# Performance work log

Measured on AMD Instinct MI355X. Metric: run time of the kernel, lower is better.

Reference implementation:

```python
import jax, jax.numpy as jnp
import numpy as np

B, D, F, K, C = 1024, 768, 24576, 64, 32  # tokens, act dim, dict size, topk, conns/feature


def setup_inputs() -> dict:
    key = jax.random.key(0)
    ks = jax.random.split(key, 9)
    s = 1.0 / np.sqrt(D)
    inp = {
        "x_up": jax.random.normal(ks[0], (B, D), jnp.float32),
        "x_down": jax.random.normal(ks[1], (B, D), jnp.float32),
        "W_enc_up": jax.random.normal(ks[2], (F, D), jnp.float32) * s,
        "b_enc_up": jnp.zeros((F,), jnp.float32),
        "W_dec_up": jax.random.normal(ks[3], (D, F), jnp.float32) * s,
        "b_dec_up": jnp.zeros((D,), jnp.float32),
        "W_enc_down": jax.random.normal(ks[4], (F, D), jnp.float32) * s,
        "b_enc_down": jnp.zeros((F,), jnp.float32),
        "W_dec_down": jax.random.normal(ks[5], (D, F), jnp.float32) * s,
        "b_dec_down": jnp.zeros((D,), jnp.float32),
    }
    # sparse adjacency: indices of connected upstream features, -1 padded
    conn = jax.random.randint(ks[6], (F, C), 0, F)
    drop = jax.random.uniform(ks[7], (F, C)) < 0.25
    inp["connections"] = jnp.where(drop, -1, conn).astype(jnp.int64)
    return inp


def _encode_topk(x, W_enc, b_enc, b_dec):
    # AutoEncoderTopK.encode: relu(Linear(x - b_dec)) then top-k, scatter to dense
    pre = jnp.maximum((x - b_dec) @ W_enc.T + b_enc, 0.0)  # [B, F]
    top_vals, top_idx = jax.lax.top_k(pre, K)              # [B, K]
    feats = jnp.zeros_like(pre).at[jnp.arange(x.shape[0])[:, None], top_idx].set(top_vals)
    return feats, top_vals, top_idx


def _decode(f, W_dec, b_dec):
    return f @ W_dec.T + b_dec


def _contributions(connections, W_dec_up, W_enc_down, up_idx, down_idx, up_vals):
    # get_virtual_weights: gather connection rows, match against active upstream
    allowed_up = connections[down_idx]                      # [B, Kd, C]
    valid = allowed_up != -1
    # match[b, kd, c, ku] = allowed_up==up_idx (masked); sum over c -> multiplicity
    match = (allowed_up[..., None] == up_idx[:, None, None, :]) & valid[..., None]
    count = match.sum(axis=2).astype(up_vals.dtype)         # [B, Kd, Ku]
    down_rows = W_enc_down[down_idx]                        # [B, Kd, D]
    up_cols = W_dec_up.T[up_idx]                            # [B, Ku, D]
    vw = jnp.einsum('bkd,bud->bku', down_rows, up_cols)     # virtual weights
    return jnp.einsum('bku,bku,bu->bk', vw, count, up_vals)  # [B, Kd]


def reference(x_up, x_down, W_enc_up, b_enc_up, W_dec_up, b_dec_up,
              W_enc_down, b_enc_down, W_dec_down, b_dec_down, connections):
    # vanilla forward (upstream recon + topk info for both)
    feats_up, up_vals, up_idx = _encode_topk(x_up, W_enc_up, b_enc_up, b_dec_up)
    recon_up = _decode(feats_up, W_dec_up, b_dec_up)
    _, down_vals, down_idx = _encode_topk(x_down, W_enc_down, b_enc_down, b_dec_down)
    # approx_forward: downstream activations approximated from virtual weights
    approx_acts = _contributions(connections, W_dec_up, W_enc_down, up_idx, down_idx, up_vals)
    approx_feats = jnp.zeros((x_down.shape[0], F), x_down.dtype).at[
        jnp.arange(x_down.shape[0])[:, None], down_idx].set(approx_acts)
    recon_down = _decode(approx_feats, W_dec_down, b_dec_down)
    return jnp.stack([recon_up, recon_down])  # [2, B, D]
```

## Files before the change

kernel.cpp:

```cpp
#include <hip/hip_runtime.h>
#include <hip/hip_bf16.h>

#define TPB 256

typedef __attribute__((ext_vector_type(4))) float f32x4;
typedef __bf16 bf16x8 __attribute__((ext_vector_type(8)));

__device__ __forceinline__ void gload16(const bf16x8* g, bf16x8* l) {
  __builtin_amdgcn_global_load_lds(
      (const __attribute__((address_space(1))) unsigned int*)g,
      (__attribute__((address_space(3))) unsigned int*)l, 16, 0, 0);
}

__device__ __forceinline__ double dot_w64(const double* xs, const float* wr,
                                          int lane, int D) {
  double sum = 0.0;
  if ((D >> 6) == 12) {
    float wv[12];
#pragma unroll
    for (int u = 0; u < 12; ++u) wv[u] = wr[lane + (u << 6)];
#pragma unroll
    for (int u = 0; u < 12; ++u) sum += xs[lane + (u << 6)] * (double)wv[u];
  } else {
    for (int d = lane; d < D; d += 64) sum += xs[d] * (double)wr[d];
  }
#pragma unroll
  for (int m = 32; m > 0; m >>= 1) sum += __shfl_xor(sum, m, 64);
  return sum;
}

__device__ __forceinline__ float dotf_w64(const float* a, const float* b,
                                          int lane, int D) {
  float s = 0.f;
  if ((D >> 6) == 12) {
    float av[12], bv[12];
#pragma unroll
    for (int u = 0; u < 12; ++u) {
      av[u] = a[lane + (u << 6)];
      bv[u] = b[lane + (u << 6)];
    }
#pragma unroll
    for (int u = 0; u < 12; ++u) s += av[u] * bv[u];
  } else {
    for (int d = lane; d < D; d += 64) s += a[d] * b[d];
  }
#pragma unroll
  for (int m = 32; m > 0; m >>= 1) s += __shfl_xor(s, m, 64);
  return s;
}

__global__ __launch_bounds__(TPB) void pack_tiles(
    const float* __restrict__ src, const float* __restrict__ sub,
    bf16x8* __restrict__ dst, int D) {
  const int r0 = blockIdx.x * 128;
  const int k0 = blockIdx.y * 32;
  const size_t tile = ((size_t)blockIdx.x * gridDim.y + blockIdx.y) * 512;
#pragma unroll
  for (int e = 0; e < 2; ++e) {
    const int q = e * 256 + threadIdx.x;
    const int row = q & 127, g = q >> 7;
    const float* s = src + (size_t)(r0 + row) * D + k0 + g * 8;
    f32x4 v0 = *(const f32x4*)s;
    f32x4 v1 = *(const f32x4*)(s + 4);
    if (sub) {
      const float* bp = sub + k0 + g * 8;
      v0 = v0 - *(const f32x4*)bp;
      v1 = v1 - *(const f32x4*)(bp + 4);
    }
    bf16x8 o;
#pragma unroll
    for (int u = 0; u < 4; ++u) o[u] = (__bf16)v0[u];
#pragma unroll
    for (int u = 0; u < 4; ++u) o[u + 4] = (__bf16)v1[u];
    dst[tile + q] = o;
  }
}

__global__ __launch_bounds__(TPB) void enc_gemm_bf(
    const bf16x8* __restrict__ A,
    const bf16x8* __restrict__ W,
    const float* __restrict__ benc,
    __bf16* __restrict__ pre,
    int nkt, int F) {
  __shared__ bf16x8 As[512], Ws[512];
  const int t = threadIdx.x;
  const int lane = t & 63, wv = t >> 6;
  const int wm = (wv >> 1) * 64, wn = (wv & 1) * 64;
  const int lrow = lane & 15, quad = lane >> 4;
  const size_t Ab = (size_t)blockIdx.y * nkt * 512;
  const size_t Wb = (size_t)blockIdx.x * nkt * 512;

  f32x4 acc[4][4];
#pragma unroll
  for (int i = 0; i < 4; ++i)
#pragma unroll
    for (int j = 0; j < 4; ++j) acc[i][j] = (f32x4){0.f, 0.f, 0.f, 0.f};

  for (int kt = 0; kt < nkt; ++kt) {
    __syncthreads();
    const bf16x8* ag = A + Ab + (size_t)kt * 512 + wv * 128;
    const bf16x8* wg = W + Wb + (size_t)kt * 512 + wv * 128;
    bf16x8* al = As + wv * 128;
    bf16x8* wl = Ws + wv * 128;
    gload16(ag + lane, al);
    gload16(ag + 64 + lane, al + 64);
    gload16(wg + lane, wl);
    gload16(wg + 64 + lane, wl + 64);
    __syncthreads();
    bf16x8 af[4];
#pragma unroll
    for (int i = 0; i < 4; ++i) af[i] = As[quad * 128 + wm + i * 16 + lrow];
#pragma unroll
    for (int j = 0; j < 4; ++j) {
      bf16x8 bfr = Ws[quad * 128 + wn + j * 16 + lrow];
#pragma unroll
      for (int i = 0; i < 4; ++i)
        acc[i][j] = __builtin_amdgcn_mfma_f32_16x16x32_bf16(af[i], bfr, acc[i][j], 0, 0, 0);
    }
  }
  const int bf0 = blockIdx.x * 128, bb = blockIdx.y * 128;
#pragma unroll
  for (int j = 0; j < 4; ++j) {
    const int col = bf0 + wn + j * 16 + lrow;
    const float bc = benc[col];
#pragma unroll
    for (int i = 0; i < 4; ++i) {
      const int row0 = bb + wm + i * 16 + quad * 4;
#pragma unroll
      for (int rg = 0; rg < 4; ++rg) {
        float v = acc[i][j][rg] + bc;
        v = v > 0.f ? v : 0.f;
        pre[(size_t)(row0 + rg) * F + col] = (__bf16)v;
      }
    }
  }
}

#define TK_CAP 2048
#define BAND_CAP 256
#define TK_EPS 0.06f

__global__ __launch_bounds__(TPB) void topk_sel(
    const unsigned short* __restrict__ pre,
    const float* __restrict__ x, const float* __restrict__ W,
    const float* __restrict__ benc, const float* __restrict__ bdec,
    float* __restrict__ vals, int* __restrict__ idxs,
    int D, int F) {
  const int b = blockIdx.x;
  const int tid = threadIdx.x;
  const unsigned short* row = pre + (size_t)b * F;

  __shared__ float cval[TK_CAP];
  __shared__ int cidx[TK_CAP];
  __shared__ unsigned hist[256];
  __shared__ double xs[768];
  __shared__ int bcand[BAND_CAP];
  __shared__ double bexact[BAND_CAP];
  __shared__ int sh_cnt, sh_out, sh_band;
  __shared__ float sh_thr;
  __shared__ unsigned sh_prefix, sh_need;

  for (int d = tid; d < D; d += TPB)
    xs[d] = (double)x[(size_t)b * D + d] - (double)bdec[d];
  if (tid == 0) sh_thr = 1.75f;
  __syncthreads();

  int n;
  float T;
  for (;;) {
    if (tid == 0) sh_cnt = 0;
    __syncthreads();
    const float thr = sh_thr;
    for (int i = tid * 8; i < F; i += TPB * 8) {
      uint4 pk = *(const uint4*)(row + i);
      unsigned wbits[4] = {pk.x, pk.y, pk.z, pk.w};
#pragma unroll
      for (int u = 0; u < 4; ++u) {
        float v0 = __uint_as_float((wbits[u] & 0xFFFFu) << 16);
        float v1 = __uint_as_float(wbits[u] & 0xFFFF0000u);
        if (v0 > thr) {
          int p = atomicAdd(&sh_cnt, 1);
          if (p < TK_CAP) { cval[p] = v0; cidx[p] = i + 2 * u; }
        }
        if (v1 > thr) {
          int p = atomicAdd(&sh_cnt, 1);
          if (p < TK_CAP) { cval[p] = v1; cidx[p] = i + 2 * u + 1; }
        }
      }
    }
    __syncthreads();
    n = sh_cnt;
    if (n >= 64 && n <= TK_CAP) {
      if (tid == 0) { sh_prefix = 0u; sh_need = 64u; }
      __syncthreads();
      for (int pass = 0; pass < 4; ++pass) {
        const int shift = 24 - 8 * pass;
        hist[tid] = 0u;
        __syncthreads();
        const unsigned prefix = sh_prefix;
        const unsigned maskhi = (pass == 0) ? 0u : (0xFFFFFFFFu << (shift + 8));
        for (int q = tid; q < n; q += TPB) {
          unsigned k = __float_as_uint(cval[q]);
          if ((k & maskhi) == prefix) atomicAdd(&hist[(k >> shift) & 255], 1u);
        }
        __syncthreads();
        if (tid == 0) {
          unsigned need = sh_need, cum = 0;
          int bsel = 0;
          for (int bin = 255; bin >= 0; --bin) {
            if (cum + hist[bin] >= need) { bsel = bin; break; }
            cum += hist[bin];
          }
          sh_prefix = prefix | ((unsigned)bsel << shift);
          sh_need = need - cum;
        }
        __syncthreads();
      }
      T = __uint_as_float(sh_prefix);
      if (thr < T - TK_EPS) break;
      if (tid == 0) sh_thr = T - 2.f * TK_EPS;
    } else {
      if (tid == 0) sh_thr = (n < 64) ? fmaxf(thr - 0.75f, 1e-3f) : thr + 0.75f;
    }
    __syncthreads();
  }

  if (tid == 0) { sh_out = 0; sh_band = 0; }
  __syncthreads();
  const float hicut = T + TK_EPS, locut = T - TK_EPS;
  float* ovals = vals + (size_t)b * 64;
  int* oidx = idxs + (size_t)b * 64;
  for (int q = tid; q < n; q += TPB) {
    const float v = cval[q];
    if (v > hicut) {
      int p = atomicAdd(&sh_out, 1);
      ovals[p] = v; oidx[p] = cidx[q];
    } else if (v >= locut) {
      int p = atomicAdd(&sh_band, 1);
      if (p < BAND_CAP) bcand[p] = cidx[q];
    }
  }
  __syncthreads();
  const int s = sh_out;
  const int bn = sh_band < BAND_CAP ? sh_band : BAND_CAP;
  const int needk = 64 - s;
  const int lane = tid & 63, wv = tid >> 6;
  for (int q = wv; q < bn; q += 4) {
    double sum = dot_w64(xs, W + (size_t)bcand[q] * D, lane, D);
    if (lane == 0) {
      double v = sum + (double)benc[bcand[q]];
      bexact[q] = v > 0.0 ? v : 0.0;
    }
  }
  __syncthreads();
  if (tid < bn) {
    const double v = bexact[tid];
    const int id = bcand[tid];
    int rank = 0;
    for (int j = 0; j < bn; ++j)
      rank += (bexact[j] > v) || (bexact[j] == v && bcand[j] < id);
    if (rank < needk) { ovals[s + rank] = (float)v; oidx[s + rank] = id; }
  }
}

__global__ __launch_bounds__(TPB) void transpose_df(
    const float* __restrict__ in, float* __restrict__ out, int D, int F) {
  __shared__ float tile[32][33];
  const int f0 = blockIdx.x * 32;
  const int d0 = blockIdx.y * 32;
  const int tx = threadIdx.x & 31;
  const int ty = threadIdx.x >> 5;
#pragma unroll
  for (int i = 0; i < 4; ++i)
    tile[ty + i * 8][tx] = in[(size_t)(d0 + ty + i * 8) * F + f0 + tx];
  __syncthreads();
#pragma unroll
  for (int i = 0; i < 4; ++i)
    out[(size_t)(f0 + ty + i * 8) * D + d0 + tx] = tile[tx][ty + i * 8];
}

__global__ __launch_bounds__(TPB) void decode64(
    const float* __restrict__ WT, const float* __restrict__ bdec,
    const float* __restrict__ vals, const int* __restrict__ idxs,
    float* __restrict__ out, int D) {
  const int b = blockIdx.x;
  __shared__ float sv[64];
  __shared__ int si[64];
  const int tid = threadIdx.x;
  if (tid < 64) {
    sv[tid] = vals[(size_t)b * 64 + tid];
    si[tid] = idxs[(size_t)b * 64 + tid];
  }
  __syncthreads();
  const int nd4 = D >> 2;
  for (int d4 = tid; d4 < nd4; d4 += TPB) {
    f32x4 acc = *(const f32x4*)(bdec + d4 * 4);
#pragma unroll 8
    for (int k = 0; k < 64; ++k)
      acc += *(const f32x4*)(WT + (size_t)si[k] * D + d4 * 4) * sv[k];
    *(f32x4*)(out + (size_t)b * D + d4 * 4) = acc;
  }
}

__global__ __launch_bounds__(TPB) void contrib(
    const int* __restrict__ conn, const float* __restrict__ Wencd,
    const float* __restrict__ WTdecu,
    const float* __restrict__ up_vals, const int* __restrict__ up_idx,
    const int* __restrict__ down_idx,
    float* __restrict__ approx, int D, int C) {
  const int b = blockIdx.x;
  __shared__ int sui[64];
  __shared__ float suv[64];
  __shared__ int sdi[64];
  __shared__ float sacc[64];
  __shared__ int queue[2048];
  __shared__ int qn;
  const int tid = threadIdx.x;
  if (tid < 64) {
    sui[tid] = up_idx[(size_t)b * 64 + tid];
    suv[tid] = up_vals[(size_t)b * 64 + tid];
    sdi[tid] = down_idx[(size_t)b * 64 + tid];
    sacc[tid] = 0.0f;
  }
  if (tid == 0) qn = 0;
  __syncthreads();
  const int npairs = 64 * C;
  for (int p = tid; p < npairs; p += TPB) {
    int kd = p / C, c = p - kd * C;
    int f = conn[(size_t)sdi[kd] * C + c];
    if (f < 0) continue;
    for (int ku = 0; ku < 64; ++ku) {
      if (sui[ku] == f) {
        int q = atomicAdd(&qn, 1);
        queue[q] = (kd << 8) | ku;
        break;
      }
    }
  }
  __syncthreads();
  const int n = qn;
  const int lane = tid & 63, wv = tid >> 6;
  for (int q = wv; q < n; q += 4) {
    const int kd = queue[q] >> 8, ku = queue[q] & 255;
    float s = dotf_w64(Wencd + (size_t)sdi[kd] * D,
                       WTdecu + (size_t)sui[ku] * D, lane, D);
    if (lane == 0) atomicAdd(&sacc[kd], suv[ku] * s);
  }
  __syncthreads();
  if (tid < 64) approx[(size_t)b * 64 + tid] = sacc[tid];
}

extern "C" void kernel_launch(void* const* d_in, const int* in_sizes, int n_in,
                              void* d_out, int out_size, void* d_ws, size_t ws_size,
                              hipStream_t stream) {
  const float* x_up   = (const float*)d_in[0];
  const float* x_down = (const float*)d_in[1];
  const float* Wenc_u = (const float*)d_in[2];
  const float* benc_u = (const float*)d_in[3];
  const float* Wdec_u = (const float*)d_in[4];
  const float* bdec_u = (const float*)d_in[5];
  const float* Wenc_d = (const float*)d_in[6];
  const float* benc_d = (const float*)d_in[7];
  const float* Wdec_d = (const float*)d_in[8];
  const float* bdec_d = (const float*)d_in[9];
  const int*   conn   = (const int*)d_in[10];

  const int D = in_sizes[5];
  const int B = in_sizes[0] / D;
  const int F = in_sizes[3];
  const int C = in_sizes[10] / F;
  const int nkt = D / 32;

  float* out = (float*)d_out;
  char* w = (char*)d_ws;

  __bf16* pre16 = (__bf16*)w;
  bf16x8* Wperm = (bf16x8*)(w + (size_t)B * F * 2);
  bf16x8* xuP   = (bf16x8*)(w + (size_t)B * F * 2 + (size_t)F * D * 2);
  bf16x8* xdP   = xuP + (size_t)B * D / 8;
  float* up_vals = (float*)(xdP + (size_t)B * D / 8);
  int*   up_idx  = (int*)(up_vals + (size_t)B * 64);
  float* dn_vals = (float*)(up_idx + (size_t)B * 64);
  int*   dn_idx  = (int*)(dn_vals + (size_t)B * 64);
  float* approx  = (float*)(dn_idx + (size_t)B * 64);
  float* WT = (float*)w;

  dim3 packW_grid(F / 128, nkt);
  dim3 packX_grid(B / 128, nkt);
  dim3 gemm_grid(F / 128, B / 128);
  dim3 tr_grid(F / 32, D / 32);

  pack_tiles<<<packX_grid, TPB, 0, stream>>>(x_up, bdec_u, xuP, D);
  pack_tiles<<<packW_grid, TPB, 0, stream>>>(Wenc_u, nullptr, Wperm, D);
  enc_gemm_bf<<<gemm_grid, TPB, 0, stream>>>(xuP, Wperm, benc_u, pre16, nkt, F);
  topk_sel<<<B, TPB, 0, stream>>>((const unsigned short*)pre16, x_up, Wenc_u,
                                  benc_u, bdec_u, up_vals, up_idx, D, F);
  pack_tiles<<<packX_grid, TPB, 0, stream>>>(x_down, bdec_d, xdP, D);
  pack_tiles<<<packW_grid, TPB, 0, stream>>>(Wenc_d, nullptr, Wperm, D);
  enc_gemm_bf<<<gemm_grid, TPB, 0, stream>>>(xdP, Wperm, benc_d, pre16, nkt, F);
  topk_sel<<<B, TPB, 0, stream>>>((const unsigned short*)pre16, x_down, Wenc_d,
                                  benc_d, bdec_d, dn_vals, dn_idx, D, F);

  transpose_df<<<tr_grid, TPB, 0, stream>>>(Wdec_u, WT, D, F);
  decode64<<<B, TPB, 0, stream>>>(WT, bdec_u, up_vals, up_idx, out, D);
  contrib<<<B, TPB, 0, stream>>>(conn, Wenc_d, WT, up_vals, up_idx, dn_idx,
                                 approx, D, C);
  transpose_df<<<tr_grid, TPB, 0, stream>>>(Wdec_d, WT, D, F);
  decode64<<<B, TPB, 0, stream>>>(WT, bdec_d, approx, dn_idx, out + (size_t)B * D, D);
}
```

Before: 693.7 us.

## Fuse top-k candidate collection into encoder GEMM epilogue

The encoder GEMM epilogue now compares each bf16 activation against a fixed threshold and appends a packed (value bits, column) word to a per-row global candidate list via atomics. The first pack kernel zeroes the counters. The top-k kernel reads that list instead of rescanning the full pre-activation row. Only if the count is out of range does it fall back to rescanning, now with a halving threshold step. The radix select uses packed keys, runs two passes instead of four, and finds the bin with a wave-level scan instead of a serial loop on one thread. This costs global atomics and scattered writes in the GEMM epilogue.

```diff
diff --git a/kernel.cpp b/kernel.cpp
--- a/kernel.cpp
+++ b/kernel.cpp
@@ -2,9 +2,17 @@
 #include <hip/hip_bf16.h>
 
 #define TPB 256
+#define TK_CAP 2048
+#define BAND_CAP 256
+#define TK_EPS 0.06f
+#define TK_THR 1.75f
 
 typedef __attribute__((ext_vector_type(4))) float f32x4;
 typedef __bf16 bf16x8 __attribute__((ext_vector_type(8)));
+
+__device__ __forceinline__ unsigned short bf16_bits(__bf16 h) {
+  return __builtin_bit_cast(unsigned short, h);
+}
 
 __device__ __forceinline__ void gload16(const bf16x8* g, bf16x8* l) {
   __builtin_amdgcn_global_load_lds(
@@ -51,7 +59,9 @@
 
 __global__ __launch_bounds__(TPB) void pack_tiles(
     const float* __restrict__ src, const float* __restrict__ sub,
-    bf16x8* __restrict__ dst, int D) {
+    bf16x8* __restrict__ dst, int D, unsigned* __restrict__ cntz, int nrows) {
+  if (cntz && blockIdx.x == 0 && blockIdx.y == 0)
+    for (int i = threadIdx.x; i < nrows; i += TPB) cntz[i] = 0u;
   const int r0 = blockIdx.x * 128;
   const int k0 = blockIdx.y * 32;
   const size_t tile = ((size_t)blockIdx.x * gridDim.y + blockIdx.y) * 512;
@@ -81,6 +91,8 @@
     const bf16x8* __restrict__ W,
     const float* __restrict__ benc,
     __bf16* __restrict__ pre,
+    unsigned* __restrict__ cnt,
+    unsigned* __restrict__ cand,
     int nkt, int F) {
   __shared__ bf16x8 As[512], Ws[512];
   const int t = threadIdx.x;
@@ -130,98 +142,133 @@
       for (int rg = 0; rg < 4; ++rg) {
         float v = acc[i][j][rg] + bc;
         v = v > 0.f ? v : 0.f;
-        pre[(size_t)(row0 + rg) * F + col] = (__bf16)v;
+        const __bf16 hb = (__bf16)v;
+        pre[(size_t)(row0 + rg) * F + col] = hb;
+        const unsigned ub = (unsigned)bf16_bits(hb);
+        const float vb = __uint_as_float(ub << 16);
+        if (vb > TK_THR) {
+          const int r = row0 + rg;
+          const unsigned p = atomicAdd(&cnt[r], 1u);
+          if (p < TK_CAP) cand[(size_t)r * TK_CAP + p] = (ub << 16) | (unsigned)col;
+        }
       }
     }
   }
 }
 
-#define TK_CAP 2048
-#define BAND_CAP 256
-#define TK_EPS 0.06f
-
-__global__ __launch_bounds__(TPB) void topk_sel(
+__global__ __launch_bounds__(TPB) void topk_sel2(
+    const unsigned* __restrict__ cnt, const unsigned* __restrict__ cand,
     const unsigned short* __restrict__ pre,
     const float* __restrict__ x, const float* __restrict__ W,
     const float* __restrict__ benc, const float* __restrict__ bdec,
-    float* __restrict__ vals, int* __restrict__ idxs,
-    int D, int F) {
+    float* __restrict__ vals, int* __restrict__ idxs, int D, int F) {
   const int b = blockIdx.x;
   const int tid = threadIdx.x;
-  const unsigned short* row = pre + (size_t)b * F;
-
-  __shared__ float cval[TK_CAP];
-  __shared__ int cidx[TK_CAP];
+
+  __shared__ unsigned cpack[TK_CAP];
   __shared__ unsigned hist[256];
   __shared__ double xs[768];
   __shared__ int bcand[BAND_CAP];
   __shared__ double bexact[BAND_CAP];
   __shared__ int sh_cnt, sh_out, sh_band;
+  __shared__ unsigned sh_prefix, sh_need;
   __shared__ float sh_thr;
-  __shared__ unsigned sh_prefix, sh_need;
 
   for (int d = tid; d < D; d += TPB)
     xs[d] = (double)x[(size_t)b * D + d] - (double)bdec[d];
-  if (tid == 0) sh_thr = 1.75f;
-  __syncthreads();
-
-  int n;
-  float T;
-  for (;;) {
-    if (tid == 0) sh_cnt = 0;
-    __syncthreads();
-    const float thr = sh_thr;
-    for (int i = tid * 8; i < F; i += TPB * 8) {
-      uint4 pk = *(const uint4*)(row + i);
-      unsigned wbits[4] = {pk.x, pk.y, pk.z, pk.w};
-#pragma unroll
-      for (int u = 0; u < 4; ++u) {
-        float v0 = __uint_as_float((wbits[u] & 0xFFFFu) << 16);
-        float v1 = __uint_as_float(wbits[u] & 0xFFFF0000u);
-        if (v0 > thr) {
-          int p = atomicAdd(&sh_cnt, 1);
-          if (p < TK_CAP) { cval[p] = v0; cidx[p] = i + 2 * u; }
+
+  int n = 0;
+  bool have = false;
+  {
+    const int nc = (int)cnt[b];
+    if (nc >= 64 && nc <= TK_CAP) {
+      for (int q = tid; q < nc; q += TPB) cpack[q] = cand[(size_t)b * TK_CAP + q];
+      n = nc;
+      have = true;
+    }
+  }
+  if (tid == 0) sh_thr = TK_THR;
+  __syncthreads();
+
+  float T = 0.f;
+  float step = 0.375f;
+  for (int outer = 0; outer < 40; ++outer) {
+    if (!have) {
+      const unsigned short* row = pre + (size_t)b * F;
+      for (int tries = 0; tries < 40; ++tries) {
+        if (tid == 0) sh_cnt = 0;
+        __syncthreads();
+        const float thr = sh_thr;
+        for (int i = tid * 8; i < F; i += TPB * 8) {
+          const uint4 pk = *(const uint4*)(row + i);
+          const unsigned wb[4] = {pk.x, pk.y, pk.z, pk.w};
+#pragma unroll
+          for (int u = 0; u < 4; ++u) {
+            const unsigned lo = wb[u] << 16;
+            const unsigned hi = wb[u] & 0xFFFF0000u;
+            if (__uint_as_float(lo) > thr) {
+              int p = atomicAdd(&sh_cnt, 1);
+              if (p < TK_CAP) cpack[p] = lo | (unsigned)(i + 2 * u);
+            }
+            if (__uint_as_float(hi) > thr) {
+              int p = atomicAdd(&sh_cnt, 1);
+              if (p < TK_CAP) cpack[p] = hi | (unsigned)(i + 2 * u + 1);
+            }
+          }
         }
-        if (v1 > thr) {
-          int p = atomicAdd(&sh_cnt, 1);
-          if (p < TK_CAP) { cval[p] = v1; cidx[p] = i + 2 * u + 1; }
+        __syncthreads();
+        n = sh_cnt;
+        if (n >= 64 && n <= TK_CAP) break;
+        if (tid == 0) sh_thr = (n < 64) ? sh_thr - step : sh_thr + step;
+        step *= 0.5f;
+        __syncthreads();
+      }
+      if (n > TK_CAP) n = TK_CAP;
+    }
+
+    if (tid == 0) { sh_prefix = 0u; sh_need = 64u; }
+#pragma unroll
+    for (int pass = 0; pass < 2; ++pass) {
+      const int shift = 24 - 8 * pass;
+      hist[tid] = 0u;
+      __syncthreads();
+      const unsigned prefix = sh_prefix;
+      const unsigned maskhi = pass == 0 ? 0u : 0xFF000000u;
+      for (int q = tid; q < n; q += TPB) {
+        const unsigned k = cpack[q];
+        if ((k & maskhi) == prefix) atomicAdd(&hist[(k >> shift) & 255u], 1u);
+      }
+      __syncthreads();
+      if (tid < 64) {
+        const unsigned h0 = hist[tid * 4], h1 = hist[tid * 4 + 1];
+        const unsigned h2 = hist[tid * 4 + 2], h3 = hist[tid * 4 + 3];
+        const unsigned lsum = h0 + h1 + h2 + h3;
+        unsigned s = lsum;
+#pragma unroll
+        for (int off = 1; off < 64; off <<= 1) {
+          const unsigned o = __shfl_down(s, off, 64);
+          if (tid + off < 64) s += o;
+        }
+        const unsigned above = s - lsum;
+        const unsigned t3 = h3, t2 = h2 + t3, t1 = h1 + t2, t0 = h0 + t1;
+        const unsigned suf[4] = {above + t0, above + t1, above + t2, above + t3};
+        const unsigned hh[4] = {h0, h1, h2, h3};
+        const unsigned need = sh_need;
+#pragma unroll
+        for (int u = 0; u < 4; ++u) {
+          if (suf[u] >= need && suf[u] - hh[u] < need) {
+            sh_prefix = prefix | ((unsigned)(tid * 4 + u) << shift);
+            sh_need = need - (suf[u] - hh[u]);
+          }
         }
       }
-    }
-    __syncthreads();
-    n = sh_cnt;
-    if (n >= 64 && n <= TK_CAP) {
-      if (tid == 0) { sh_prefix = 0u; sh_need = 64u; }
       __syncthreads();
-      for (int pass = 0; pass < 4; ++pass) {
-        const int shift = 24 - 8 * pass;
-        hist[tid] = 0u;
-        __syncthreads();
-        const unsigned prefix = sh_prefix;
-        const unsigned maskhi = (pass == 0) ? 0u : (0xFFFFFFFFu << (shift + 8));
-        for (int q = tid; q < n; q += TPB) {
-          unsigned k = __float_as_uint(cval[q]);
-          if ((k & maskhi) == prefix) atomicAdd(&hist[(k >> shift) & 255], 1u);
-        }
-        __syncthreads();
-        if (tid == 0) {
-          unsigned need = sh_need, cum = 0;
-          int bsel = 0;
-          for (int bin = 255; bin >= 0; --bin) {
-            if (cum + hist[bin] >= need) { bsel = bin; break; }
-            cum += hist[bin];
-          }
-          sh_prefix = prefix | ((unsigned)bsel << shift);
-          sh_need = need - cum;
-        }
-        __syncthreads();
-      }
-      T = __uint_as_float(sh_prefix);
-      if (thr < T - TK_EPS) break;
-      if (tid == 0) sh_thr = T - 2.f * TK_EPS;
-    } else {
-      if (tid == 0) sh_thr = (n < 64) ? fmaxf(thr - 0.75f, 1e-3f) : thr + 0.75f;
-    }
+    }
+    T = __uint_as_float(sh_prefix);
+    const float colthr = sh_thr;
+    if (colthr < T - TK_EPS) break;
+    have = false;
+    if (tid == 0) sh_thr = T - 2.f * TK_EPS;
     __syncthreads();
   }
 
@@ -231,13 +278,15 @@
   float* ovals = vals + (size_t)b * 64;
   int* oidx = idxs + (size_t)b * 64;
   for (int q = tid; q < n; q += TPB) {
-    const float v = cval[q];
+    const unsigned k = cpack[q];
+    const float v = __uint_as_float(k & 0xFFFF0000u);
+    const int id = (int)(k & 0xFFFFu);
     if (v > hicut) {
       int p = atomicAdd(&sh_out, 1);
-      ovals[p] = v; oidx[p] = cidx[q];
+      ovals[p] = v; oidx[p] = id;
     } else if (v >= locut) {
       int p = atomicAdd(&sh_band, 1);
-      if (p < BAND_CAP) bcand[p] = cidx[q];
+      if (p < BAND_CAP) bcand[p] = id;
     }
   }
   __syncthreads();
@@ -383,6 +432,8 @@
   float* dn_vals = (float*)(up_idx + (size_t)B * 64);
   int*   dn_idx  = (int*)(dn_vals + (size_t)B * 64);
   float* approx  = (float*)(dn_idx + (size_t)B * 64);
+  unsigned* cnt  = (unsigned*)(approx + (size_t)B * 64);
+  unsigned* cand = cnt + B;
   float* WT = (float*)w;
 
   dim3 packW_grid(F / 128, nkt);
@@ -390,16 +441,16 @@
   dim3 gemm_grid(F / 128, B / 128);
   dim3 tr_grid(F / 32, D / 32);
 
-  pack_tiles<<<packX_grid, TPB, 0, stream>>>(x_up, bdec_u, xuP, D);
-  pack_tiles<<<packW_grid, TPB, 0, stream>>>(Wenc_u, nullptr, Wperm, D);
-  enc_gemm_bf<<<gemm_grid, TPB, 0, stream>>>(xuP, Wperm, benc_u, pre16, nkt, F);
-  topk_sel<<<B, TPB, 0, stream>>>((const unsigned short*)pre16, x_up, Wenc_u,
-                                  benc_u, bdec_u, up_vals, up_idx, D, F);
-  pack_tiles<<<packX_grid, TPB, 0, stream>>>(x_down, bdec_d, xdP, D);
-  pack_tiles<<<packW_grid, TPB, 0, stream>>>(Wenc_d, nullptr, Wperm, D);
-  enc_gemm_bf<<<gemm_grid, TPB, 0, stream>>>(xdP, Wperm, benc_d, pre16, nkt, F);
-  topk_sel<<<B, TPB, 0, stream>>>((const unsigned short*)pre16, x_down, Wenc_d,
-                                  benc_d, bdec_d, dn_vals, dn_idx, D, F);
+  pack_tiles<<<packX_grid, TPB, 0, stream>>>(x_up, bdec_u, xuP, D, cnt, B);
+  pack_tiles<<<packW_grid, TPB, 0, stream>>>(Wenc_u, nullptr, Wperm, D, nullptr, 0);
+  enc_gemm_bf<<<gemm_grid, TPB, 0, stream>>>(xuP, Wperm, benc_u, pre16, cnt, cand, nkt, F);
+  topk_sel2<<<B, TPB, 0, stream>>>(cnt, cand, (const unsigned short*)pre16, x_up,
+                                   Wenc_u, benc_u, bdec_u, up_vals, up_idx, D, F);
+  pack_tiles<<<packX_grid, TPB, 0, stream>>>(x_down, bdec_d, xdP, D, cnt, B);
+  pack_tiles<<<packW_grid, TPB, 0, stream>>>(Wenc_d, nullptr, Wperm, D, nullptr, 0);
+  enc_gemm_bf<<<gemm_grid, TPB, 0, stream>>>(xdP, Wperm, benc_d, pre16, cnt, cand, nkt, F);
+  topk_sel2<<<B, TPB, 0, stream>>>(cnt, cand, (const unsigned short*)pre16, x_down,
+                                   Wenc_d, benc_d, bdec_d, dn_vals, dn_idx, D, F);
 
   transpose_df<<<tr_grid, TPB, 0, stream>>>(Wdec_u, WT, D, F);
   decode64<<<B, TPB, 0, stream>>>(WT, bdec_u, up_vals, up_idx, out, D);
```

Result: slower. 1.523 ms (+119.6%).
